# Optimization experiments

Measured on AMD Instinct MI355X. Metric: run time of the kernel, lower is better.

## Reference

```python
import jax, jax.numpy as jnp
import numpy as np
import math

B = 128          # batch
D = 512          # d_model
H = 8            # n_heads
L = 6            # n_layers
S = 200          # max_len (fixed by temporal bias table)
LAT = 256        # style_latent_dim + skill_latent_dim
OUT = 6          # output_dim
DK = D // H
DFF = 4 * D


def _ln(x, g, b):
    # torch LayerNorm, eps=1e-5
    mu = jnp.mean(x, axis=-1, keepdims=True)
    var = jnp.mean((x - mu) ** 2, axis=-1, keepdims=True)
    return (x - mu) / jnp.sqrt(var + 1e-5) * g + b


def _gelu(x):
    # torch nn.GELU default = exact (erf) gelu
    return jax.nn.gelu(x, approximate=False)


def setup_inputs() -> dict:
    key = jax.random.key(0)
    ks = iter(jax.random.split(key, 16))
    n = lambda shape: jax.random.normal(next(ks), shape, jnp.float32) * 0.02
    # deterministic temporal bias: bias[i,j] = -0.1*|i-j|/S, shared across heads
    t = jnp.arange(S, dtype=jnp.float32)
    tb = (-0.1 * jnp.abs(t[:, None] - t[None, :]) / S).astype(jnp.float32)
    temp_bias = jnp.broadcast_to(tb, (1, H, S, S)) + 0.0
    inp = {
        'z_style': jax.random.normal(next(ks), (B, 128), jnp.float32),
        'z_skill': jax.random.normal(next(ks), (B, 128), jnp.float32),
        'W_lat': n((LAT, D * S)), 'b_lat': jnp.zeros((D * S,), jnp.float32),
        'temp_bias': temp_bias,
        'Wq': n((L, D, D)), 'bq': jnp.zeros((L, D), jnp.float32),
        'Wk': n((L, D, D)), 'bk': jnp.zeros((L, D), jnp.float32),
        'Wv': n((L, D, D)), 'bv': jnp.zeros((L, D), jnp.float32),
        'Wo': n((L, D, D)), 'bo': jnp.zeros((L, D), jnp.float32),
        'g1': jnp.ones((L, D), jnp.float32), 'be1': jnp.zeros((L, D), jnp.float32),
        'g2': jnp.ones((L, D), jnp.float32), 'be2': jnp.zeros((L, D), jnp.float32),
        'W1': n((L, D, DFF)), 'bf1': jnp.zeros((L, DFF), jnp.float32),
        'W2': n((L, DFF, D)), 'bf2': jnp.zeros((L, D), jnp.float32),
        'Wp1': n((D, D // 2)), 'bp1': jnp.zeros((D // 2,), jnp.float32),
        'Wp2': n((D // 2, OUT)), 'bp2': jnp.zeros((OUT,), jnp.float32),
        'Ws1': n((LAT, D // 2)), 'bs1': jnp.zeros((D // 2,), jnp.float32),
        'Ws2': n((D // 2, 5)), 'bs2': jnp.zeros((5,), jnp.float32),
    }
    return inp


def reference(z_style, z_skill, W_lat, b_lat, temp_bias, Wq, bq, Wk, bk, Wv, bv,
              Wo, bo, g1, be1, g2, be2, W1, bf1, W2, bf2, Wp1, bp1, Wp2, bp2,
              Ws1, bs1, Ws2, bs2):
    z = jnp.concatenate([z_style, z_skill], axis=1)          # [B, LAT]
    x = _gelu(z @ W_lat + b_lat).reshape(-1, S, D)           # [B, S, D]
    # sinusoidal positional encoding (buffer)
    pos = jnp.arange(S, dtype=jnp.float32)[:, None]
    div = jnp.exp(jnp.arange(0, D, 2, dtype=jnp.float32) * (-math.log(10000.0) / D))
    pe = jnp.zeros((S, D), jnp.float32)
    pe = pe.at[:, 0::2].set(jnp.sin(pos * div)).at[:, 1::2].set(jnp.cos(pos * div))
    x = x + pe[None]
    scale = math.sqrt(DK)
    for l in range(L):
        q = (x @ Wq[l] + bq[l]).reshape(-1, S, H, DK)
        k = (x @ Wk[l] + bk[l]).reshape(-1, S, H, DK)
        v = (x @ Wv[l] + bv[l]).reshape(-1, S, H, DK)
        scores = jnp.einsum('bihd,bjhd->bhij', q, k) / scale + temp_bias  # [B,H,S,S]
        w = jax.nn.softmax(scores, axis=-1)
        ctx = jnp.einsum('bhij,bjhd->bihd', w, v).reshape(-1, S, D)
        attn = ctx @ Wo[l] + bo[l]
        x = _ln(x + attn, g1[l], be1[l])
        ff = _gelu(x @ W1[l] + bf1[l]) @ W2[l] + bf2[l]
        x = _ln(x + ff, g2[l], be2[l])
    trajectory = _gelu(x @ Wp1 + bp1) @ Wp2 + bp2            # [B, S, OUT]
    signatures = _gelu(z @ Ws1 + bs1) @ Ws2 + bs2            # [B, 5]
    return trajectory, signatures
```

## Files before the change

### kernel.cpp

```cpp
#include <hip/hip_runtime.h>
#include <math.h>

#define BATCH 128
#define DMODEL 512
#define NHEAD 8
#define NLAYER 6
#define SEQ 200
#define LATDIM 256
#define OUTDIM 6
#define DFF 2048
#define ROWS (BATCH * SEQ)
#define QKVS 1536
#define VTS 264

typedef unsigned short u16;
typedef __attribute__((ext_vector_type(8))) short bfrag8;
typedef __attribute__((ext_vector_type(4))) float facc4;

__device__ __forceinline__ float gelu_f(float v) {
    const float x = v * 0.70710678118654752f;
    const float ax = fabsf(x);
    const float t = __builtin_amdgcn_rcpf(fmaf(0.3275911f, ax, 1.0f));
    float p = fmaf(1.061405429f, t, -1.453152027f);
    p = fmaf(p, t, 1.421413741f);
    p = fmaf(p, t, -0.284496736f);
    p = fmaf(p, t, 0.254829592f);
    p = p * t;
    const float e = __expf(-ax * ax);
    float er = fmaf(-p, e, 1.0f);
    er = copysignf(er, x);
    return 0.5f * v * (1.0f + er);
}
__device__ __forceinline__ u16 f2bf(float f) {
    unsigned u = __float_as_uint(f);
    u += 0x7fffu + ((u >> 16) & 1u);
    return (u16)(u >> 16);
}
__device__ __forceinline__ void gl_lds16(const u16* g, u16* l) {
    __builtin_amdgcn_global_load_lds(
        (const __attribute__((address_space(1))) void*)(uintptr_t)g,
        (__attribute__((address_space(3))) void*)(uintptr_t)l,
        16, 0, 0);
}

enum { MM_QKV = 0, MM_RESID = 1, MM_GELU_BF16 = 2, MM_GELU_F32 = 3, MM_LAT = 4 };

__global__ __launch_bounds__(256) void mm_kernel(
    const u16* __restrict__ A, const u16* __restrict__ Bt,
    const float* __restrict__ bias, float* __restrict__ Cf, u16* __restrict__ Cb,
    const float* __restrict__ pe, int M, int N, int K, int mode, int gx)
{
    __shared__ __align__(16) u16 As[3 * 4096];
    __shared__ __align__(16) u16 Bs[3 * 4096];
    const int tid = threadIdx.x;

    const unsigned nwg = gridDim.x, cpx = nwg >> 3;
    const unsigned id = blockIdx.x;
    const unsigned swz = (id & 7u) * cpx + (id >> 3);
    const int bx = (int)(swz % (unsigned)gx);
    const int by = (int)(swz / (unsigned)gx);
    const int row0 = by * 128, col0 = bx * 128;

    const int lane = tid & 63, w = tid >> 6;
    const int m_w = (w & 1) << 6, n_w = (w >> 1) << 6;
    const int l16 = lane & 15, quad = lane >> 4;

    const int r0 = tid >> 2;
    const int seg = ((tid & 3) ^ ((tid >> 3) & 3)) << 3;
    const u16* Ag0 = A + (size_t)(row0 + r0) * K + seg;
    const u16* Ag1 = A + (size_t)(row0 + r0 + 64) * K + seg;
    const u16* Bg0 = Bt + (size_t)(col0 + r0) * K + seg;
    const u16* Bg1 = Bt + (size_t)(col0 + r0 + 64) * K + seg;

    const int pos = (quad ^ ((l16 >> 1) & 3)) << 3;

    facc4 acc[4][4] = {};
    const int iters = K >> 5;

    u16* Ald = As + w * 512;
    u16* Bld = Bs + w * 512;
    #pragma unroll
    for (int pf = 0; pf < 3; ++pf) {
        const int ko = pf << 5;
        const int bo = pf << 12;
        gl_lds16(Ag0 + ko, Ald + bo);
        gl_lds16(Ag1 + ko, Ald + bo + 2048);
        gl_lds16(Bg0 + ko, Bld + bo);
        gl_lds16(Bg1 + ko, Bld + bo + 2048);
    }

    int b = 0;
    for (int it = 0; it < iters; ++it) {
        const int ahead = iters - 1 - it;
        if (ahead >= 2)      asm volatile("s_waitcnt vmcnt(8)" ::: "memory");
        else if (ahead == 1) asm volatile("s_waitcnt vmcnt(4)" ::: "memory");
        else                 asm volatile("s_waitcnt vmcnt(0)" ::: "memory");
        __builtin_amdgcn_s_barrier();
        asm volatile("" ::: "memory");

        const u16* Ab = As + (b << 12);
        const u16* Bb = Bs + (b << 12);
        bfrag8 af[4], bf[4];
        #pragma unroll
        for (int i = 0; i < 4; ++i)
            af[i] = *(const bfrag8*)&Ab[(m_w + i * 16 + l16) * 32 + pos];
        #pragma unroll
        for (int j = 0; j < 4; ++j)
            bf[j] = *(const bfrag8*)&Bb[(n_w + j * 16 + l16) * 32 + pos];
        __builtin_amdgcn_s_setprio(1);
        #pragma unroll
        for (int i = 0; i < 4; ++i)
            #pragma unroll
            for (int j = 0; j < 4; ++j)
                acc[i][j] = __builtin_amdgcn_mfma_f32_16x16x32_bf16(
                    af[i], bf[j], acc[i][j], 0, 0, 0);
        __builtin_amdgcn_s_setprio(0);

        __builtin_amdgcn_sched_barrier(0);
        asm volatile("" ::: "memory");
        __builtin_amdgcn_s_barrier();
        asm volatile("" ::: "memory");

        if (it + 3 < iters) {
            const int ko = (it + 3) << 5;
            const int bo = b << 12;
            gl_lds16(Ag0 + ko, Ald + bo);
            gl_lds16(Ag1 + ko, Ald + bo + 2048);
            gl_lds16(Bg0 + ko, Bld + bo);
            gl_lds16(Bg1 + ko, Bld + bo + 2048);
        }
        b = (b == 2) ? 0 : b + 1;
    }

    #pragma unroll
    for (int i = 0; i < 4; ++i) {
        #pragma unroll
        for (int r = 0; r < 4; ++r) {
            const int row = row0 + m_w + i * 16 + quad * 4 + r;
            #pragma unroll
            for (int j = 0; j < 4; ++j) {
                const int col = col0 + n_w + j * 16 + l16;
                float v = acc[i][j][r] + bias[col];
                const size_t idx = (size_t)row * N + col;
                if (mode == MM_QKV) {
                    Cb[idx] = f2bf(v);
                } else if (mode == MM_RESID) {
                    Cf[idx] += v;
                } else if (mode == MM_GELU_BF16) {
                    Cb[idx] = f2bf(gelu_f(v));
                } else if (mode == MM_GELU_F32) {
                    Cf[idx] = gelu_f(v);
                } else {
                    v = gelu_f(v) + pe[col];
                    Cf[idx] = v;
                    Cb[idx] = f2bf(v);
                }
            }
        }
    }
}

__global__ __launch_bounds__(512) void mm256_kernel(
    const u16* __restrict__ A, const u16* __restrict__ Bt,
    const float* __restrict__ bias, float* __restrict__ Cf, u16* __restrict__ Cb,
    int N, int K, int mode, int gx)
{
    __shared__ __align__(16) u16 As[3 * 8192];
    __shared__ __align__(16) u16 Bs[3 * 4096];
    const int tid = threadIdx.x;

    const unsigned nwg = gridDim.x, cpx = nwg >> 3;
    const unsigned id = blockIdx.x;
    const unsigned swz = (id & 7u) * cpx + (id >> 3);
    const int bx = (int)(swz % (unsigned)gx);
    const int by = (int)(swz / (unsigned)gx);
    const int row0 = by * 256, col0 = bx * 128;

    const int lane = tid & 63, w = tid >> 6;
    const int m_w = (w & 3) << 6, n_w = (w >> 2) << 6;
    const int l16 = lane & 15, quad = lane >> 4;

    const int r0 = tid >> 2;
    const int seg = ((tid & 3) ^ ((tid >> 3) & 3)) << 3;
    const u16* Ag0 = A + (size_t)(row0 + r0) * K + seg;
    const u16* Ag1 = A + (size_t)(row0 + r0 + 128) * K + seg;
    const u16* Bg0 = Bt + (size_t)(col0 + r0) * K + seg;

    const int pos = (quad ^ ((l16 >> 1) & 3)) << 3;

    facc4 acc[4][4] = {};
    const int iters = K >> 5;

    u16* Ald = As + w * 512;
    u16* Bld = Bs + w * 512;
    #pragma unroll
    for (int pf = 0; pf < 3; ++pf) {
        const int ko = pf << 5;
        gl_lds16(Ag0 + ko, Ald + pf * 8192);
        gl_lds16(Ag1 + ko, Ald + pf * 8192 + 4096);
        gl_lds16(Bg0 + ko, Bld + pf * 4096);
    }

    int b = 0;
    for (int it = 0; it < iters; ++it) {
        const int ahead = iters - 1 - it;
        if (ahead >= 2)      asm volatile("s_waitcnt vmcnt(6)" ::: "memory");
        else if (ahead == 1) asm volatile("s_waitcnt vmcnt(3)" ::: "memory");
        else                 asm volatile("s_waitcnt vmcnt(0)" ::: "memory");
        __builtin_amdgcn_s_barrier();
        asm volatile("" ::: "memory");

        const u16* Ab = As + b * 8192;
        const u16* Bb = Bs + b * 4096;
        bfrag8 af[4], bf[4];
        #pragma unroll
        for (int i = 0; i < 4; ++i)
            af[i] = *(const bfrag8*)&Ab[(m_w + i * 16 + l16) * 32 + pos];
        #pragma unroll
        for (int j = 0; j < 4; ++j)
            bf[j] = *(const bfrag8*)&Bb[(n_w + j * 16 + l16) * 32 + pos];
        __builtin_amdgcn_s_setprio(1);
        #pragma unroll
        for (int i = 0; i < 4; ++i)
            #pragma unroll
            for (int j = 0; j < 4; ++j)
                acc[i][j] = __builtin_amdgcn_mfma_f32_16x16x32_bf16(
                    af[i], bf[j], acc[i][j], 0, 0, 0);
        __builtin_amdgcn_s_setprio(0);

        __builtin_amdgcn_sched_barrier(0);
        asm volatile("" ::: "memory");
        __builtin_amdgcn_s_barrier();
        asm volatile("" ::: "memory");

        if (it + 3 < iters) {
            const int ko = (it + 3) << 5;
            gl_lds16(Ag0 + ko, Ald + b * 8192);
            gl_lds16(Ag1 + ko, Ald + b * 8192 + 4096);
            gl_lds16(Bg0 + ko, Bld + b * 4096);
        }
        b = (b == 2) ? 0 : b + 1;
    }

    #pragma unroll
    for (int i = 0; i < 4; ++i) {
        #pragma unroll
        for (int r = 0; r < 4; ++r) {
            const int row = row0 + m_w + i * 16 + quad * 4 + r;
            #pragma unroll
            for (int j = 0; j < 4; ++j) {
                const int col = col0 + n_w + j * 16 + l16;
                float v = acc[i][j][r] + bias[col];
                const size_t idx = (size_t)row * N + col;
                if (mode == MM_QKV)        Cb[idx] = f2bf(v);
                else if (mode == MM_RESID) Cf[idx] += v;
                else                       Cb[idx] = f2bf(gelu_f(v));
            }
        }
    }
}

__global__ __launch_bounds__(256) void pe_kernel(float* __restrict__ pe)
{
    const int idx = blockIdx.x * 256 + threadIdx.x;
    const int s = idx >> 9, d = idx & 511;
    const float ang = (float)s * expf((float)(d & ~1) * (-9.2103403719761836f / 512.0f));
    pe[idx] = (d & 1) ? cosf(ang) : sinf(ang);
}

__global__ __launch_bounds__(256) void attn_kernel(
    const u16* __restrict__ qkv, const float* __restrict__ tb,
    u16* __restrict__ ctxb)
{
    const int qt = blockIdx.x, h = blockIdx.y, b = blockIdx.z;
    const int tid = threadIdx.x;
    const int w = tid >> 6, lane = tid & 63;
    const int l16 = lane & 15, quad = lane >> 4;

    __shared__ __align__(16) u16 kv[16896];
    __shared__ __align__(16) u16 Ps[4][16][232];

    const size_t rowbase = (size_t)b * SEQ;
    const int q0w = qt * 64 + w * 16;

    for (int g = w; g < 26; g += 4) {
        const int c = g * 64 + lane;
        const int key = c >> 3, seg = c & 7;
        const int krow = key < 200 ? key : 199;
        gl_lds16(qkv + (rowbase + krow) * QKVS + 512 + h * 64 +
                 ((seg ^ (key & 7)) << 3),
                 kv + g * 512);
    }
    int qrow = (int)rowbase + q0w + l16;
    if (qrow > ROWS - 1) qrow = ROWS - 1;
    const u16* qp = qkv + (size_t)qrow * QKVS + h * 64 + quad * 8;
    bfrag8 aq0 = *(const bfrag8*)(qp);
    bfrag8 aq1 = *(const bfrag8*)(qp + 32);
    __syncthreads();

    facc4 sc[13];
    #pragma unroll
    for (int nt = 0; nt < 13; ++nt) {
        const int key = nt * 16 + l16, kk = key & 7;
        bfrag8 b0 = *(const bfrag8*)&kv[key * 64 + ((quad ^ kk) << 3)];
        bfrag8 b1 = *(const bfrag8*)&kv[key * 64 + (((4 + quad) ^ kk) << 3)];
        facc4 a = {};
        a = __builtin_amdgcn_mfma_f32_16x16x32_bf16(aq0, b0, a, 0, 0, 0);
        a = __builtin_amdgcn_mfma_f32_16x16x32_bf16(aq1, b1, a, 0, 0, 0);
        sc[nt] = a;
    }
    __syncthreads();

    for (int c = 0; c < 7; ++c) {
        const int key = c * 32 + (tid & 31);
        const int dkb = (tid >> 5) * 8;
        u16 vals[8];
        if (key < 200) {
            *(uint4*)vals = *(const uint4*)(qkv + (rowbase + key) * QKVS +
                                            1024 + h * 64 + dkb);
        } else {
            #pragma unroll
            for (int i = 0; i < 8; ++i) vals[i] = 0;
        }
        #pragma unroll
        for (int i = 0; i < 8; ++i)
            kv[(dkb + i) * VTS + key] = vals[i];
    }

    #pragma unroll
    for (int r = 0; r < 4; ++r) {
        const int i = q0w + quad * 4 + r;
        #pragma unroll
        for (int nt = 0; nt < 13; ++nt) {
            const int j = nt * 16 + l16;
            float s;
            if (j < 200) {
                const float tbv = (i < 200) ? tb[(h * 200 + i) * 200 + j] : 0.f;
                s = sc[nt][r] * 0.125f + tbv;
            } else s = -INFINITY;
            sc[nt][r] = s;
        }
        float m = sc[0][r];
        #pragma unroll
        for (int nt = 1; nt < 13; ++nt) m = fmaxf(m, sc[nt][r]);
        #pragma unroll
        for (int off = 8; off > 0; off >>= 1) m = fmaxf(m, __shfl_xor(m, off, 64));
        float ssum = 0.f;
        #pragma unroll
        for (int nt = 0; nt < 13; ++nt) {
            const float e = __expf(sc[nt][r] - m);
            sc[nt][r] = e; ssum += e;
        }
        #pragma unroll
        for (int off = 8; off > 0; off >>= 1) ssum += __shfl_xor(ssum, off, 64);
        const float inv = 1.0f / ssum;
        #pragma unroll
        for (int nt = 0; nt < 13; ++nt)
            Ps[w][quad * 4 + r][nt * 16 + l16] = f2bf(sc[nt][r] * inv);
        Ps[w][quad * 4 + r][208 + l16] = 0;
    }
    __syncthreads();

    facc4 pacc[4] = {};
    for (int ks = 0; ks < 7; ++ks) {
        bfrag8 ap = *(const bfrag8*)&Ps[w][l16][ks * 32 + quad * 8];
        #pragma unroll
        for (int nt = 0; nt < 4; ++nt) {
            const int dkrow = nt * 16 + l16;
            bfrag8 bv = *(const bfrag8*)&kv[dkrow * VTS + ks * 32 + quad * 8];
            pacc[nt] = __builtin_amdgcn_mfma_f32_16x16x32_bf16(ap, bv, pacc[nt], 0, 0, 0);
        }
    }

    #pragma unroll
    for (int r = 0; r < 4; ++r) {
        const int i = q0w + quad * 4 + r;
        if (i < 200) {
            #pragma unroll
            for (int nt = 0; nt < 4; ++nt)
                ctxb[(rowbase + i) * 512 + h * 64 + nt * 16 + l16] = f2bf(pacc[nt][r]);
        }
    }
}

__global__ __launch_bounds__(256) void tconv_kernel(
    const float* __restrict__ W, u16* __restrict__ O, int K, int N,
    size_t wStride, size_t oStride)
{
    __shared__ u16 T[64][80];
    const float* Wz = W + wStride * blockIdx.z;
    u16* Oz = O + oStride * blockIdx.z;
    const int n0 = blockIdx.x * 64, k0 = blockIdx.y * 64, t = threadIdx.x;
    {
        const int kr = t >> 2, seg = t & 3;
        const float* wp = Wz + (size_t)(k0 + kr) * N + n0 + seg * 16;
        alignas(16) u16 tmp[16];
        #pragma unroll
        for (int q = 0; q < 4; ++q) {
            float4 f = ((const float4*)wp)[q];
            tmp[q * 4 + 0] = f2bf(f.x); tmp[q * 4 + 1] = f2bf(f.y);
            tmp[q * 4 + 2] = f2bf(f.z); tmp[q * 4 + 3] = f2bf(f.w);
        }
        *(uint4*)&T[kr][seg * 16]     = *(uint4*)&tmp[0];
        *(uint4*)&T[kr][seg * 16 + 8] = *(uint4*)&tmp[8];
    }
    __syncthreads();
    {
        const int n = t >> 2, kseg = t & 3;
        alignas(16) u16 o[16];
        #pragma unroll
        for (int i = 0; i < 16; ++i) o[i] = T[kseg * 16 + i][n];
        uint4* op = (uint4*)(Oz + (size_t)(n0 + n) * K + k0 + kseg * 16);
        op[0] = *(uint4*)&o[0];
        op[1] = *(uint4*)&o[8];
    }
}

__global__ __launch_bounds__(256) void tconv4_kernel(
    const float* __restrict__ Wq, const float* __restrict__ Wk,
    const float* __restrict__ Wv, const float* __restrict__ Wo,
    u16* __restrict__ Out)
{
    __shared__ u16 T[64][80];
    const int z = blockIdx.z, layer = z >> 2, m = z & 3;
    const float* W = (m == 0 ? Wq : m == 1 ? Wk : m == 2 ? Wv : Wo)
                     + (size_t)layer * 262144;
    u16* O = Out + (size_t)z * 262144;
    const int n0 = blockIdx.x * 64, k0 = blockIdx.y * 64, t = threadIdx.x;
    {
        const int kr = t >> 2, seg = t & 3;
        const float* wp = W + (size_t)(k0 + kr) * 512 + n0 + seg * 16;
        alignas(16) u16 tmp[16];
        #pragma unroll
        for (int q = 0; q < 4; ++q) {
            float4 f = ((const float4*)wp)[q];
            tmp[q * 4 + 0] = f2bf(f.x); tmp[q * 4 + 1] = f2bf(f.y);
            tmp[q * 4 + 2] = f2bf(f.z); tmp[q * 4 + 3] = f2bf(f.w);
        }
        *(uint4*)&T[kr][seg * 16]     = *(uint4*)&tmp[0];
        *(uint4*)&T[kr][seg * 16 + 8] = *(uint4*)&tmp[8];
    }
    __syncthreads();
    {
        const int n = t >> 2, kseg = t & 3;
        alignas(16) u16 o[16];
        #pragma unroll
        for (int i = 0; i < 16; ++i) o[i] = T[kseg * 16 + i][n];
        uint4* op = (uint4*)(O + (size_t)(n0 + n) * 512 + k0 + kseg * 16);
        op[0] = *(uint4*)&o[0];
        op[1] = *(uint4*)&o[8];
    }
}

__global__ __launch_bounds__(256) void bqkv_kernel(
    const float* __restrict__ bq, const float* __restrict__ bk,
    const float* __restrict__ bv, float* __restrict__ o)
{
    const int l = blockIdx.x, t = threadIdx.x;
    for (int c = t; c < 1536; c += 256) {
        float v = (c < 512) ? bq[l * 512 + c]
                : (c < 1024) ? bk[l * 512 + c - 512]
                             : bv[l * 512 + c - 1024];
        o[l * 1536 + c] = v;
    }
}

__global__ __launch_bounds__(256) void ln_kernel(
    float* __restrict__ x, const float* __restrict__ g,
    const float* __restrict__ bb, u16* __restrict__ xb)
{
    const int w = threadIdx.x >> 6, lane = threadIdx.x & 63;
    const size_t row = (size_t)blockIdx.x * 4 + w;
    float* xr = x + row * DMODEL;
    u16* xbr = xb + row * DMODEL;
    const int c = lane * 8;
    float4 a = *(const float4*)(xr + c);
    float4 b = *(const float4*)(xr + c + 4);
    float s = a.x + a.y + a.z + a.w + b.x + b.y + b.z + b.w;
    #pragma unroll
    for (int off = 32; off > 0; off >>= 1) s += __shfl_xor(s, off, 64);
    const float mu = s * (1.0f / 512.0f);
    a.x -= mu; a.y -= mu; a.z -= mu; a.w -= mu;
    b.x -= mu; b.y -= mu; b.z -= mu; b.w -= mu;
    float v = a.x * a.x + a.y * a.y + a.z * a.z + a.w * a.w
            + b.x * b.x + b.y * b.y + b.z * b.z + b.w * b.w;
    #pragma unroll
    for (int off = 32; off > 0; off >>= 1) v += __shfl_xor(v, off, 64);
    const float rstd = rsqrtf(v * (1.0f / 512.0f) + 1e-5f);
    float4 g0 = *(const float4*)(g + c), g1 = *(const float4*)(g + c + 4);
    float4 b0 = *(const float4*)(bb + c), b1 = *(const float4*)(bb + c + 4);
    float4 o0, o1;
    o0.x = a.x * rstd * g0.x + b0.x; o0.y = a.y * rstd * g0.y + b0.y;
    o0.z = a.z * rstd * g0.z + b0.z; o0.w = a.w * rstd * g0.w + b0.w;
    o1.x = b.x * rstd * g1.x + b1.x; o1.y = b.y * rstd * g1.y + b1.y;
    o1.z = b.z * rstd * g1.z + b1.z; o1.w = b.w * rstd * g1.w + b1.w;
    *(float4*)(xr + c) = o0;
    *(float4*)(xr + c + 4) = o1;
    alignas(16) u16 ob[8] = { f2bf(o0.x), f2bf(o0.y), f2bf(o0.z), f2bf(o0.w),
                              f2bf(o1.x), f2bf(o1.y), f2bf(o1.z), f2bf(o1.w) };
    *(uint4*)(xbr + c) = *(uint4*)ob;
}

__global__ __launch_bounds__(256) void concat_z_kernel(
    const float* __restrict__ zs, const float* __restrict__ zk, u16* __restrict__ z)
{
    const int b = blockIdx.x, t = threadIdx.x;
    z[b * 256 + t] = f2bf((t < 128) ? zs[b * 128 + t] : zk[b * 128 + t - 128]);
}

__global__ __launch_bounds__(64) void traj_head_kernel(
    const float* __restrict__ t1, const float* __restrict__ Wp2,
    const float* __restrict__ bp2, float* __restrict__ out)
{
    const int r = blockIdx.x, t = threadIdx.x;
    __shared__ float red[6][64];
    float p[6] = {};
    const float* tr = t1 + (size_t)r * 256;
    for (int kk = t; kk < 256; kk += 64) {
        float tv = tr[kk];
        #pragma unroll
        for (int c = 0; c < 6; ++c) p[c] = fmaf(tv, Wp2[kk * 6 + c], p[c]);
    }
    #pragma unroll
    for (int c = 0; c < 6; ++c) red[c][t] = p[c];
    __syncthreads();
    if (t < 6) {
        float a = 0.f;
        for (int j = 0; j < 64; ++j) a += red[t][j];
        out[(size_t)r * 6 + t] = a + bp2[t];
    }
}

__global__ __launch_bounds__(256) void sig_head_kernel(
    const float* __restrict__ zs, const float* __restrict__ zk,
    const float* __restrict__ Ws1, const float* __restrict__ bs1,
    const float* __restrict__ Ws2, const float* __restrict__ bs2,
    float* __restrict__ out)
{
    const int b = blockIdx.x, t = threadIdx.x;
    __shared__ float zrow[256];
    __shared__ float h1[256];
    zrow[t] = (t < 128) ? zs[b * 128 + t] : zk[b * 128 + t - 128];
    __syncthreads();
    float acc = bs1[t];
    for (int kk = 0; kk < 256; ++kk) acc = fmaf(zrow[kk], Ws1[kk * 256 + t], acc);
    h1[t] = gelu_f(acc);
    __syncthreads();
    if (t < 5) {
        float a = bs2[t];
        for (int kk = 0; kk < 256; ++kk) a = fmaf(h1[kk], Ws2[kk * 5 + t], a);
        out[b * 5 + t] = a;
    }
}

extern "C" void kernel_launch(void* const* d_in, const int* in_sizes, int n_in,
                              void* d_out, int out_size, void* d_ws, size_t ws_size,
                              hipStream_t stream) {
    const float* z_style   = (const float*)d_in[0];
    const float* z_skill   = (const float*)d_in[1];
    const float* W_lat     = (const float*)d_in[2];
    const float* b_lat     = (const float*)d_in[3];
    const float* temp_bias = (const float*)d_in[4];
    const float* Wq  = (const float*)d_in[5];
    const float* bq  = (const float*)d_in[6];
    const float* Wk  = (const float*)d_in[7];
    const float* bk  = (const float*)d_in[8];
    const float* Wv  = (const float*)d_in[9];
    const float* bv  = (const float*)d_in[10];
    const float* Wo  = (const float*)d_in[11];
    const float* bo  = (const float*)d_in[12];
    const float* g1  = (const float*)d_in[13];
    const float* be1 = (const float*)d_in[14];
    const float* g2  = (const float*)d_in[15];
    const float* be2 = (const float*)d_in[16];
    const float* W1  = (const float*)d_in[17];
    const float* bf1 = (const float*)d_in[18];
    const float* W2  = (const float*)d_in[19];
    const float* bf2 = (const float*)d_in[20];
    const float* Wp1 = (const float*)d_in[21];
    const float* bp1 = (const float*)d_in[22];
    const float* Wp2 = (const float*)d_in[23];
    const float* bp2 = (const float*)d_in[24];
    const float* Ws1 = (const float*)d_in[25];
    const float* bs1 = (const float*)d_in[26];
    const float* Ws2 = (const float*)d_in[27];
    const float* bs2 = (const float*)d_in[28];
    float* out = (float*)d_out;

    char* Wb = (char*)d_ws;
    float* x     = (float*)(Wb + 0);
    u16*  xb     = (u16*)(Wb + 52428800);
    u16*  qkv    = (u16*)(Wb + 78643200);
    u16*  cx     = (u16*)(Wb + 157286400);
    u16*  ff1b   = (u16*)(Wb + 78643200);
    u16*  wlatT  = (u16*)(Wb + 78643200);
    float* t1    = (float*)(Wb + 157286400);
    u16*  qkvoT  = (u16*)(Wb + 183500800);
    u16*  w1T    = (u16*)(Wb + 196083712);
    u16*  w2T    = (u16*)(Wb + 208666624);
    u16*  wp1T   = (u16*)(Wb + 221249536);
    float* bqkv  = (float*)(Wb + 221511680);
    u16*  zbb    = (u16*)(Wb + 221548544);
    float* pe    = (float*)(Wb + 221614080);

    tconv4_kernel<<<dim3(8, 8, 24), 256, 0, stream>>>(Wq, Wk, Wv, Wo, qkvoT);
    tconv_kernel<<<dim3(32, 8, 6), 256, 0, stream>>>(W1, w1T, DMODEL, DFF,
                                                     (size_t)DMODEL * DFF, (size_t)DMODEL * DFF);
    tconv_kernel<<<dim3(8, 32, 6), 256, 0, stream>>>(W2, w2T, DFF, DMODEL,
                                                     (size_t)DMODEL * DFF, (size_t)DMODEL * DFF);
    tconv_kernel<<<dim3(1600, 4, 1), 256, 0, stream>>>(W_lat, wlatT, LATDIM, DMODEL * SEQ, 0, 0);
    tconv_kernel<<<dim3(4, 8, 1), 256, 0, stream>>>(Wp1, wp1T, DMODEL, 256, 0, 0);
    bqkv_kernel<<<NLAYER, 256, 0, stream>>>(bq, bk, bv, bqkv);
    concat_z_kernel<<<BATCH, 256, 0, stream>>>(z_style, z_skill, zbb);
    pe_kernel<<<400, 256, 0, stream>>>(pe);

    mm_kernel<<<dim3(800), 256, 0, stream>>>(
        zbb, wlatT, b_lat, x, xb, pe, BATCH, DMODEL * SEQ, LATDIM, MM_LAT, 800);

    for (int l = 0; l < NLAYER; ++l) {
        mm256_kernel<<<dim3(12 * 100), 512, 0, stream>>>(
            xb, qkvoT + (size_t)l * 4 * 262144, bqkv + l * 1536, nullptr, qkv,
            QKVS, DMODEL, MM_QKV, 12);
        attn_kernel<<<dim3(4, NHEAD, BATCH), 256, 0, stream>>>(qkv, temp_bias, cx);
        mm256_kernel<<<dim3(4 * 100), 512, 0, stream>>>(
            cx, qkvoT + (size_t)(l * 4 + 3) * 262144, bo + l * DMODEL, x, nullptr,
            DMODEL, DMODEL, MM_RESID, 4);
        ln_kernel<<<ROWS / 4, 256, 0, stream>>>(x, g1 + l * DMODEL, be1 + l * DMODEL, xb);
        mm256_kernel<<<dim3(16 * 100), 512, 0, stream>>>(
            xb, w1T + (size_t)l * DMODEL * DFF, bf1 + l * DFF, nullptr, ff1b,
            DFF, DMODEL, MM_GELU_BF16, 16);
        mm256_kernel<<<dim3(4 * 100), 512, 0, stream>>>(
            ff1b, w2T + (size_t)l * DMODEL * DFF, bf2 + l * DMODEL, x, nullptr,
            DMODEL, DFF, MM_RESID, 4);
        ln_kernel<<<ROWS / 4, 256, 0, stream>>>(x, g2 + l * DMODEL, be2 + l * DMODEL, xb);
    }

    mm_kernel<<<dim3(2 * 200), 256, 0, stream>>>(
        xb, wp1T, bp1, t1, nullptr, pe, ROWS, 256, DMODEL, MM_GELU_F32, 2);
    traj_head_kernel<<<ROWS, 64, 0, stream>>>(t1, Wp2, bp2, out);
    sig_head_kernel<<<BATCH, 256, 0, stream>>>(z_style, z_skill, Ws1, bs1, Ws2, bs2,
                                               out + (size_t)ROWS * OUTDIM);
}
```

Baseline: 2.941 ms.

## Use packed bf16 conversion, simplify GELU, hoist epilogue bias, template LDS buffering

Replaces scalar float-to-bf16 rounding with the hardware v_cvt_pk_bf16_f32 instruction in GEMM epilogues, attention, layernorm and weight conversion. Rewrites the erf-based GELU with pre-halved coefficients so it needs fewer operations and no copysign. Hoists the bias and positional-encoding loads out of the epilogue loops. Templates the small GEMM on pipeline depth so the latent projection (K=256) uses two LDS buffers instead of three. These are mostly instruction-count trims in epilogues and are small relative to the MFMA work, and the new conversion may round differently from the old manual round-to-nearest-even code.

```diff
diff --git a/kernel.cpp b/kernel.cpp
--- a/kernel.cpp
+++ b/kernel.cpp
@@ -17,19 +17,23 @@
 typedef __attribute__((ext_vector_type(8))) short bfrag8;
 typedef __attribute__((ext_vector_type(4))) float facc4;
 
+__device__ __forceinline__ unsigned cvt_pk_bf16(float lo, float hi) {
+    unsigned r;
+    asm("v_cvt_pk_bf16_f32 %0, %1, %2" : "=v"(r) : "v"(lo), "v"(hi));
+    return r;
+}
 __device__ __forceinline__ float gelu_f(float v) {
-    const float x = v * 0.70710678118654752f;
-    const float ax = fabsf(x);
+    const float av = fabsf(v);
+    const float ax = av * 0.70710678118654752f;
     const float t = __builtin_amdgcn_rcpf(fmaf(0.3275911f, ax, 1.0f));
-    float p = fmaf(1.061405429f, t, -1.453152027f);
-    p = fmaf(p, t, 1.421413741f);
-    p = fmaf(p, t, -0.284496736f);
-    p = fmaf(p, t, 0.254829592f);
+    float p = fmaf(0.5305027145f, t, -0.7265760135f);
+    p = fmaf(p, t, 0.7107068705f);
+    p = fmaf(p, t, -0.142248368f);
+    p = fmaf(p, t, 0.127414796f);
     p = p * t;
     const float e = __expf(-ax * ax);
-    float er = fmaf(-p, e, 1.0f);
-    er = copysignf(er, x);
-    return 0.5f * v * (1.0f + er);
+    const float er05 = fmaf(-p, e, 0.5f);
+    return fmaf(av, er05, 0.5f * v);
 }
 __device__ __forceinline__ u16 f2bf(float f) {
     unsigned u = __float_as_uint(f);
@@ -45,13 +49,14 @@
 
 enum { MM_QKV = 0, MM_RESID = 1, MM_GELU_BF16 = 2, MM_GELU_F32 = 3, MM_LAT = 4 };
 
+template<int NBUF>
 __global__ __launch_bounds__(256) void mm_kernel(
     const u16* __restrict__ A, const u16* __restrict__ Bt,
     const float* __restrict__ bias, float* __restrict__ Cf, u16* __restrict__ Cb,
     const float* __restrict__ pe, int M, int N, int K, int mode, int gx)
 {
-    __shared__ __align__(16) u16 As[3 * 4096];
-    __shared__ __align__(16) u16 Bs[3 * 4096];
+    __shared__ __align__(16) u16 As[NBUF * 4096];
+    __shared__ __align__(16) u16 Bs[NBUF * 4096];
     const int tid = threadIdx.x;
 
     const unsigned nwg = gridDim.x, cpx = nwg >> 3;
@@ -80,7 +85,7 @@
     u16* Ald = As + w * 512;
     u16* Bld = Bs + w * 512;
     #pragma unroll
-    for (int pf = 0; pf < 3; ++pf) {
+    for (int pf = 0; pf < NBUF; ++pf) {
         const int ko = pf << 5;
         const int bo = pf << 12;
         gl_lds16(Ag0 + ko, Ald + bo);
@@ -92,9 +97,14 @@
     int b = 0;
     for (int it = 0; it < iters; ++it) {
         const int ahead = iters - 1 - it;
-        if (ahead >= 2)      asm volatile("s_waitcnt vmcnt(8)" ::: "memory");
-        else if (ahead == 1) asm volatile("s_waitcnt vmcnt(4)" ::: "memory");
-        else                 asm volatile("s_waitcnt vmcnt(0)" ::: "memory");
+        if constexpr (NBUF == 3) {
+            if (ahead >= 2)      asm volatile("s_waitcnt vmcnt(8)" ::: "memory");
+            else if (ahead == 1) asm volatile("s_waitcnt vmcnt(4)" ::: "memory");
+            else                 asm volatile("s_waitcnt vmcnt(0)" ::: "memory");
+        } else {
+            if (ahead >= 1)      asm volatile("s_waitcnt vmcnt(4)" ::: "memory");
+            else                 asm volatile("s_waitcnt vmcnt(0)" ::: "memory");
+        }
         __builtin_amdgcn_s_barrier();
         asm volatile("" ::: "memory");
 
@@ -121,15 +131,23 @@
         __builtin_amdgcn_s_barrier();
         asm volatile("" ::: "memory");
 
-        if (it + 3 < iters) {
-            const int ko = (it + 3) << 5;
+        if (it + NBUF < iters) {
+            const int ko = (it + NBUF) << 5;
             const int bo = b << 12;
             gl_lds16(Ag0 + ko, Ald + bo);
             gl_lds16(Ag1 + ko, Ald + bo + 2048);
             gl_lds16(Bg0 + ko, Bld + bo);
             gl_lds16(Bg1 + ko, Bld + bo + 2048);
         }
-        b = (b == 2) ? 0 : b + 1;
+        b = (b == NBUF - 1) ? 0 : b + 1;
+    }
+
+    float bv[4], pev[4];
+    #pragma unroll
+    for (int j = 0; j < 4; ++j) bv[j] = bias[col0 + n_w + j * 16 + l16];
+    if (mode == MM_LAT) {
+        #pragma unroll
+        for (int j = 0; j < 4; ++j) pev[j] = pe[col0 + n_w + j * 16 + l16];
     }
 
     #pragma unroll
@@ -137,24 +155,38 @@
         #pragma unroll
         for (int r = 0; r < 4; ++r) {
             const int row = row0 + m_w + i * 16 + quad * 4 + r;
+            const size_t base = (size_t)row * N + col0 + n_w + l16;
+            float v[4];
             #pragma unroll
-            for (int j = 0; j < 4; ++j) {
-                const int col = col0 + n_w + j * 16 + l16;
-                float v = acc[i][j][r] + bias[col];
-                const size_t idx = (size_t)row * N + col;
-                if (mode == MM_QKV) {
-                    Cb[idx] = f2bf(v);
-                } else if (mode == MM_RESID) {
-                    Cf[idx] += v;
-                } else if (mode == MM_GELU_BF16) {
-                    Cb[idx] = f2bf(gelu_f(v));
-                } else if (mode == MM_GELU_F32) {
-                    Cf[idx] = gelu_f(v);
-                } else {
-                    v = gelu_f(v) + pe[col];
-                    Cf[idx] = v;
-                    Cb[idx] = f2bf(v);
+            for (int j = 0; j < 4; ++j) v[j] = acc[i][j][r] + bv[j];
+            if (mode == MM_QKV) {
+                const unsigned p01 = cvt_pk_bf16(v[0], v[1]);
+                const unsigned p23 = cvt_pk_bf16(v[2], v[3]);
+                Cb[base]      = (u16)p01; Cb[base + 16] = (u16)(p01 >> 16);
+                Cb[base + 32] = (u16)p23; Cb[base + 48] = (u16)(p23 >> 16);
+            } else if (mode == MM_RESID) {
+                #pragma unroll
+                for (int j = 0; j < 4; ++j) Cf[base + j * 16] += v[j];
+            } else if (mode == MM_GELU_BF16) {
+                #pragma unroll
+                for (int j = 0; j < 4; ++j) v[j] = gelu_f(v[j]);
+                const unsigned p01 = cvt_pk_bf16(v[0], v[1]);
+                const unsigned p23 = cvt_pk_bf16(v[2], v[3]);
+                Cb[base]      = (u16)p01; Cb[base + 16] = (u16)(p01 >> 16);
+                Cb[base + 32] = (u16)p23; Cb[base + 48] = (u16)(p23 >> 16);
+            } else if (mode == MM_GELU_F32) {
+                #pragma unroll
+                for (int j = 0; j < 4; ++j) Cf[base + j * 16] = gelu_f(v[j]);
+            } else {
+                #pragma unroll
+                for (int j = 0; j < 4; ++j) {
+                    v[j] = gelu_f(v[j]) + pev[j];
+                    Cf[base + j * 16] = v[j];
                 }
+                const unsigned p01 = cvt_pk_bf16(v[0], v[1]);
+                const unsigned p23 = cvt_pk_bf16(v[2], v[3]);
+                Cb[base]      = (u16)p01; Cb[base + 16] = (u16)(p01 >> 16);
+                Cb[base + 32] = (u16)p23; Cb[base + 48] = (u16)(p23 >> 16);
             }
         }
     }
@@ -242,19 +274,31 @@
         b = (b == 2) ? 0 : b + 1;
     }
 
+    float bv[4];
+    #pragma unroll
+    for (int j = 0; j < 4; ++j) bv[j] = bias[col0 + n_w + j * 16 + l16];
+
     #pragma unroll
     for (int i = 0; i < 4; ++i) {
         #pragma unroll
         for (int r = 0; r < 4; ++r) {
             const int row = row0 + m_w + i * 16 + quad * 4 + r;
+            const size_t base = (size_t)row * N + col0 + n_w + l16;
+            float v[4];
             #pragma unroll
-            for (int j = 0; j < 4; ++j) {
-                const int col = col0 + n_w + j * 16 + l16;
-                float v = acc[i][j][r] + bias[col];
-                const size_t idx = (size_t)row * N + col;
-                if (mode == MM_QKV)        Cb[idx] = f2bf(v);
-                else if (mode == MM_RESID) Cf[idx] += v;
-                else                       Cb[idx] = f2bf(gelu_f(v));
+            for (int j = 0; j < 4; ++j) v[j] = acc[i][j][r] + bv[j];
+            if (mode == MM_RESID) {
+                #pragma unroll
+                for (int j = 0; j < 4; ++j) Cf[base + j * 16] += v[j];
+            } else {
+                if (mode == MM_GELU_BF16) {
+                    #pragma unroll
+                    for (int j = 0; j < 4; ++j) v[j] = gelu_f(v[j]);
+                }
+                const unsigned p01 = cvt_pk_bf16(v[0], v[1]);
+                const unsigned p23 = cvt_pk_bf16(v[2], v[3]);
+                Cb[base]      = (u16)p01; Cb[base + 16] = (u16)(p01 >> 16);
+                Cb[base + 32] = (u16)p23; Cb[base + 48] = (u16)(p23 >> 16);
             }
         }
     }
@@ -354,10 +398,15 @@
         #pragma unroll
         for (int off = 8; off > 0; off >>= 1) ssum += __shfl_xor(ssum, off, 64);
         const float inv = 1.0f / ssum;
-        #pragma unroll
-        for (int nt = 0; nt < 13; ++nt)
-            Ps[w][quad * 4 + r][nt * 16 + l16] = f2bf(sc[nt][r] * inv);
-        Ps[w][quad * 4 + r][208 + l16] = 0;
+        u16* psr = &Ps[w][quad * 4 + r][0];
+        #pragma unroll
+        for (int nt = 0; nt < 12; nt += 2) {
+            const unsigned pq = cvt_pk_bf16(sc[nt][r] * inv, sc[nt + 1][r] * inv);
+            psr[nt * 16 + l16]       = (u16)pq;
+            psr[(nt + 1) * 16 + l16] = (u16)(pq >> 16);
+        }
+        psr[192 + l16] = f2bf(sc[12][r] * inv);
+        psr[208 + l16] = 0;
     }
     __syncthreads();
 
@@ -376,9 +425,11 @@
     for (int r = 0; r < 4; ++r) {
         const int i = q0w + quad * 4 + r;
         if (i < 200) {
-            #pragma unroll
-            for (int nt = 0; nt < 4; ++nt)
-                ctxb[(rowbase + i) * 512 + h * 64 + nt * 16 + l16] = f2bf(pacc[nt][r]);
+            const unsigned p01 = cvt_pk_bf16(pacc[0][r], pacc[1][r]);
+            const unsigned p23 = cvt_pk_bf16(pacc[2][r], pacc[3][r]);
+            u16* cp = ctxb + (rowbase + i) * 512 + h * 64 + l16;
+            cp[0]  = (u16)p01; cp[16] = (u16)(p01 >> 16);
+            cp[32] = (u16)p23; cp[48] = (u16)(p23 >> 16);
         }
     }
 }
@@ -394,15 +445,15 @@
     {
         const int kr = t >> 2, seg = t & 3;
         const float* wp = Wz + (size_t)(k0 + kr) * N + n0 + seg * 16;
-        alignas(16) u16 tmp[16];
+        alignas(16) unsigned tmp[8];
         #pragma unroll
         for (int q = 0; q < 4; ++q) {
             float4 f = ((const float4*)wp)[q];
-            tmp[q * 4 + 0] = f2bf(f.x); tmp[q * 4 + 1] = f2bf(f.y);
-            tmp[q * 4 + 2] = f2bf(f.z); tmp[q * 4 + 3] = f2bf(f.w);
+            tmp[q * 2]     = cvt_pk_bf16(f.x, f.y);
+            tmp[q * 2 + 1] = cvt_pk_bf16(f.z, f.w);
         }
         *(uint4*)&T[kr][seg * 16]     = *(uint4*)&tmp[0];
-        *(uint4*)&T[kr][seg * 16 + 8] = *(uint4*)&tmp[8];
+        *(uint4*)&T[kr][seg * 16 + 8] = *(uint4*)&tmp[4];
     }
     __syncthreads();
     {
@@ -430,15 +481,15 @@
     {
         const int kr = t >> 2, seg = t & 3;
         const float* wp = W + (size_t)(k0 + kr) * 512 + n0 + seg * 16;
-        alignas(16) u16 tmp[16];
+        alignas(16) unsigned tmp[8];
         #pragma unroll
         for (int q = 0; q < 4; ++q) {
             float4 f = ((const float4*)wp)[q];
-            tmp[q * 4 + 0] = f2bf(f.x); tmp[q * 4 + 1] = f2bf(f.y);
-            tmp[q * 4 + 2] = f2bf(f.z); tmp[q * 4 + 3] = f2bf(f.w);
+            tmp[q * 2]     = cvt_pk_bf16(f.x, f.y);
+            tmp[q * 2 + 1] = cvt_pk_bf16(f.z, f.w);
         }
         *(uint4*)&T[kr][seg * 16]     = *(uint4*)&tmp[0];
-        *(uint4*)&T[kr][seg * 16 + 8] = *(uint4*)&tmp[8];
+        *(uint4*)&T[kr][seg * 16 + 8] = *(uint4*)&tmp[4];
     }
     __syncthreads();
     {
@@ -496,9 +547,12 @@
     o1.z = b.z * rstd * g1.z + b1.z; o1.w = b.w * rstd * g1.w + b1.w;
     *(float4*)(xr + c) = o0;
     *(float4*)(xr + c + 4) = o1;
-    alignas(16) u16 ob[8] = { f2bf(o0.x), f2bf(o0.y), f2bf(o0.z), f2bf(o0.w),
-                              f2bf(o1.x), f2bf(o1.y), f2bf(o1.z), f2bf(o1.w) };
-    *(uint4*)(xbr + c) = *(uint4*)ob;
+    uint4 ob;
+    ob.x = cvt_pk_bf16(o0.x, o0.y);
+    ob.y = cvt_pk_bf16(o0.z, o0.w);
+    ob.z = cvt_pk_bf16(o1.x, o1.y);
+    ob.w = cvt_pk_bf16(o1.z, o1.w);
+    *(uint4*)(xbr + c) = ob;
 }
 
 __global__ __launch_bounds__(256) void concat_z_kernel(
@@ -614,7 +668,7 @@
     concat_z_kernel<<<BATCH, 256, 0, stream>>>(z_style, z_skill, zbb);
     pe_kernel<<<400, 256, 0, stream>>>(pe);
 
-    mm_kernel<<<dim3(800), 256, 0, stream>>>(
+    mm_kernel<2><<<dim3(800), 256, 0, stream>>>(
         zbb, wlatT, b_lat, x, xb, pe, BATCH, DMODEL * SEQ, LATDIM, MM_LAT, 800);
 
     for (int l = 0; l < NLAYER; ++l) {
@@ -635,7 +689,7 @@
         ln_kernel<<<ROWS / 4, 256, 0, stream>>>(x, g2 + l * DMODEL, be2 + l * DMODEL, xb);
     }
 
-    mm_kernel<<<dim3(2 * 200), 256, 0, stream>>>(
+    mm_kernel<3><<<dim3(2 * 200), 256, 0, stream>>>(
         xb, wp1T, bp1, t1, nullptr, pe, ROWS, 256, DMODEL, MM_GELU_F32, 2);
     traj_head_kernel<<<ROWS, 64, 0, stream>>>(t1, Wp2, bp2, out);
     sig_head_kernel<<<BATCH, 256, 0, stream>>>(z_style, z_skill, Ws1, bs1, Ws2, bs2,
```

New measurement: 2.580 ms. 12.3% less time.
